# Kernel optimization log

Hardware: AMD Instinct MI355X
Metric: run time of the kernel (lower is better)

The kernel has to match this reference:

```python
import jax, jax.numpy as jnp
import numpy as np


def setup_inputs() -> dict:
    B, N, D, M = 512, 128, 768, 32  # bags, num_class, embed_dim, max bag size
    rng = np.random.default_rng(0)
    sizes = rng.integers(8, 25, size=B)  # variable bag sizes in [8, 24], all <= M
    offsets = np.concatenate([[0], np.cumsum(sizes)]).astype(np.int32)
    nsum = int(offsets[-1])
    scope = np.stack([offsets[:-1], offsets[1:]], axis=1)  # (B, 2) [start, end)

    key = jax.random.key(0)
    k1, k2, k3 = jax.random.split(key, 3)
    rep = jax.random.normal(k1, (nsum, D), dtype=jnp.float32)
    fc_weight = jax.random.normal(k2, (N, D), dtype=jnp.float32) * 0.02
    fc_bias = jax.random.normal(k3, (N,), dtype=jnp.float32) * 0.02
    return {
        "rep": rep,
        "fc_weight": fc_weight,
        "fc_bias": fc_bias,
        "scope": jnp.asarray(scope),
        "max_bag": M,
    }


def reference(rep, fc_weight, fc_bias, scope, max_bag):
    """IntraBagAttention forward (train=False, bag_size=0 branch), ragged bags
    rewritten as padded/masked dense ops.

    rep:       (nsum, D) sentence-encoder outputs
    fc_weight: (N, D), fc_bias: (N,)
    scope:     (B, 2) int [start, end) per bag; max_bag: static int pad bound
    returns:   (B, N) per-relation bag scores
    """
    nsum = rep.shape[0]
    starts = scope[:, 0]
    sizes = scope[:, 1] - scope[:, 0]
    pos = jnp.arange(max_bag)
    idx = jnp.clip(starts[:, None] + pos[None, :], 0, nsum - 1)  # (B, M)
    valid = pos[None, :] < sizes[:, None]                        # (B, M)
    bag = rep[idx]                                               # (B, M, D)

    # att_score = rep @ fc.weight.data.T ; .data => no grad through this use
    w_att = jax.lax.stop_gradient(fc_weight)
    att = jnp.einsum('bmd,nd->bnm', bag, w_att)                  # (B, N, M)
    att = jnp.where(valid[:, None, :], att, -jnp.inf)
    sm = jax.nn.softmax(att, axis=-1)                            # per-bag softmax over sentences

    # weighted segment sum: one attended rep per relation per bag
    rfer = jnp.einsum('bnm,bmd->bnd', sm, bag)                   # (B, N, D)

    # fc(rep_for_each_rel) -> (B, N, N); softmax over classes; take diagonal
    full = jnp.einsum('bnd,kd->bnk', rfer, fc_weight) + fc_bias  # (B, N, N)
    probs = jax.nn.softmax(full, axis=-1)
    return jnp.diagonal(probs, axis1=1, axis2=2)                 # (B, N)
```

## Files before the change

kernel.cpp:

```cpp
#include <hip/hip_runtime.h>
#include <math.h>

#define B_BAGS 512
#define N_REL  128
#define D_DIM  768
#define NCHUNK 4

typedef __attribute__((ext_vector_type(8))) short  bf16x8;
typedef __attribute__((ext_vector_type(4))) float  f32x4;

__device__ inline unsigned pack_hi(float f0, float f1) {
    return __builtin_amdgcn_perm(__float_as_uint(f1), __float_as_uint(f0), 0x07060302u);
}
__device__ inline float trunc_res(float f) {
    return f - __uint_as_float(__float_as_uint(f) & 0xFFFF0000u);
}

__global__ void build_bfrag(const float* __restrict__ W, unsigned* __restrict__ Bfrag) {
    int flat = blockIdx.x * 256 + threadIdx.x;
    int lane = flat & 63;
    int tile = (flat >> 6) & 7;
    int s    = flat >> 9;
    int n  = tile * 16 + (lane & 15);
    int k0 = s * 32 + (lane >> 4) * 8;
    const float* src = &W[n * D_DIM + k0];
    float f[8];
    #pragma unroll
    for (int j = 0; j < 8; ++j) f[j] = src[j];
    unsigned hi[4], lo[4];
    #pragma unroll
    for (int q = 0; q < 4; ++q) {
        hi[q] = pack_hi(f[2*q], f[2*q+1]);
        lo[q] = pack_hi(trunc_res(f[2*q]), trunc_res(f[2*q+1]));
    }
    unsigned base = (unsigned)(((s * 8 + tile) * 2) * 64 + lane) * 4;
    *(uint4*)&Bfrag[base]          = make_uint4(hi[0], hi[1], hi[2], hi[3]);
    *(uint4*)&Bfrag[base + 64 * 4] = make_uint4(lo[0], lo[1], lo[2], lo[3]);
}

__global__ __launch_bounds__(512, 2) void h_gemm(
    const float*    __restrict__ rep,
    const unsigned* __restrict__ Bfrag,
    float*          __restrict__ Hp,
    int nsum, int hstride)
{
    __shared__ unsigned As[2 * 128 * 36];

    const int t     = threadIdx.x;
    const int strip = blockIdx.x;
    const int chunk = blockIdx.y;

    const int wv   = t >> 6;
    const int lane = t & 63;
    const int nl15 = lane & 15;
    const int lg   = lane >> 4;
    const int j    = wv & 3;
    const int nh   = wv >> 2;

    const int srow = t >> 2;
    const int scq  = t & 3;
    int grow = strip * 128 + srow;
    grow = (grow > nsum - 1) ? (nsum - 1) : grow;
    const float* srp = &rep[(size_t)grow * D_DIM + chunk * 192 + scq * 16];

    f32x4 acc[2][4][2];
    #pragma unroll
    for (int mt = 0; mt < 2; ++mt)
        #pragma unroll
        for (int i = 0; i < 4; ++i) {
            acc[mt][i][0] = f32x4{0.f, 0.f, 0.f, 0.f};
            acc[mt][i][1] = f32x4{0.f, 0.f, 0.f, 0.f};
        }

    unsigned afo[2][2];
    #pragma unroll
    for (int mt = 0; mt < 2; ++mt) {
        const int row = (j * 2 + mt) * 16 + nl15;
        afo[mt][0] = (0 * 128 + row) * 36 + lg * 4;
        afo[mt][1] = (1 * 128 + row) * 36 + lg * 4;
    }

    #pragma unroll
    for (int st = 0; st < 3; ++st) {
        if (st) __syncthreads();
        {
            const float4 v0 = *(const float4*)&srp[st * 64];
            const float4 v1 = *(const float4*)&srp[st * 64 + 4];
            const float4 v2 = *(const float4*)&srp[st * 64 + 8];
            const float4 v3 = *(const float4*)&srp[st * 64 + 12];
            unsigned hi[8], lo[8];
            const float f[16] = {v0.x,v0.y,v0.z,v0.w, v1.x,v1.y,v1.z,v1.w,
                                 v2.x,v2.y,v2.z,v2.w, v3.x,v3.y,v3.z,v3.w};
            #pragma unroll
            for (int w = 0; w < 8; ++w) {
                hi[w] = pack_hi(f[2*w], f[2*w+1]);
                lo[w] = pack_hi(trunc_res(f[2*w]), trunc_res(f[2*w+1]));
            }
            const unsigned bh = (0 * 128 + srow) * 36 + scq * 8;
            const unsigned bl = (1 * 128 + srow) * 36 + scq * 8;
            *(uint4*)&As[bh]     = make_uint4(hi[0], hi[1], hi[2], hi[3]);
            *(uint4*)&As[bh + 4] = make_uint4(hi[4], hi[5], hi[6], hi[7]);
            *(uint4*)&As[bl]     = make_uint4(lo[0], lo[1], lo[2], lo[3]);
            *(uint4*)&As[bl + 4] = make_uint4(lo[4], lo[5], lo[6], lo[7]);
        }
        __syncthreads();

        #pragma unroll
        for (int g = 0; g < 2; ++g) {
            const int gsg = chunk * 6 + st * 2 + g;
            bf16x8 ah[2], al[2];
            #pragma unroll
            for (int mt = 0; mt < 2; ++mt) {
                ah[mt] = *(const bf16x8*)&As[afo[mt][0] + g * 16];
                al[mt] = *(const bf16x8*)&As[afo[mt][1] + g * 16];
            }
            #pragma unroll
            for (int i = 0; i < 4; ++i) {
                const int nt = nh * 4 + i;
                const bf16x8 bh = *(const bf16x8*)&Bfrag[((gsg * 8 + nt) * 2 + 0) * 256 + lane * 4];
                const bf16x8 bl = *(const bf16x8*)&Bfrag[((gsg * 8 + nt) * 2 + 1) * 256 + lane * 4];
                #pragma unroll
                for (int mt = 0; mt < 2; ++mt) {
                    acc[mt][i][0] = __builtin_amdgcn_mfma_f32_16x16x32_bf16(ah[mt], bh, acc[mt][i][0], 0, 0, 0);
                    acc[mt][i][1] = __builtin_amdgcn_mfma_f32_16x16x32_bf16(ah[mt], bl, acc[mt][i][1], 0, 0, 0);
                    acc[mt][i][1] = __builtin_amdgcn_mfma_f32_16x16x32_bf16(al[mt], bh, acc[mt][i][1], 0, 0, 0);
                }
            }
        }
    }

    float* H = Hp + (size_t)chunk * hstride;
    #pragma unroll
    for (int mt = 0; mt < 2; ++mt) {
        const int rowb = strip * 128 + (j * 2 + mt) * 16 + lg * 4;
        #pragma unroll
        for (int i = 0; i < 4; ++i) {
            const int col = (nh * 4 + i) * 16 + nl15;
            #pragma unroll
            for (int r = 0; r < 4; ++r)
                H[(size_t)(rowb + r) * N_REL + col] = acc[mt][i][0][r] + acc[mt][i][1][r];
        }
    }
}

__global__ __launch_bounds__(512, 2) void bag_out(
    const float* __restrict__ Hp, int hstride,
    const float* __restrict__ bias,
    const int*   __restrict__ scope,
    float*       __restrict__ out,
    int nsum)
{
    __shared__ unsigned Gfrag[8 * 2 * 64 * 4];
    __shared__ unsigned SMfrag[8 * 2 * 64 * 4];

    const int t = threadIdx.x;
    const int b = blockIdx.x;
    const int start = scope[2 * b];
    const int size  = scope[2 * b + 1] - start;

    const int wv   = t >> 6;
    const int lane = t & 63;
    const int nl15 = lane & 15;
    const int lg   = lane >> 4;
    const int T    = wv;

    float gv[2][4], smv[2][4];
    #pragma unroll
    for (int mt = 0; mt < 2; ++mt)
        #pragma unroll
        for (int r = 0; r < 4; ++r) {
            int row = start + mt * 16 + lg * 4 + r;
            row = (row > nsum - 1) ? (nsum - 1) : row;
            const float* p = &Hp[(size_t)row * N_REL + T * 16 + nl15];
            gv[mt][r] = p[0] + p[(size_t)hstride] + p[(size_t)hstride * 2]
                             + p[(size_t)hstride * 3];
        }

    float vmax = -INFINITY;
    #pragma unroll
    for (int mt = 0; mt < 2; ++mt)
        #pragma unroll
        for (int r = 0; r < 4; ++r) {
            const int m = mt * 16 + lg * 4 + r;
            if (m < size) vmax = fmaxf(vmax, gv[mt][r]);
        }
    vmax = fmaxf(vmax, __shfl_xor(vmax, 16));
    vmax = fmaxf(vmax, __shfl_xor(vmax, 32));

    float ssum = 0.f;
    #pragma unroll
    for (int mt = 0; mt < 2; ++mt)
        #pragma unroll
        for (int r = 0; r < 4; ++r) {
            const int m = mt * 16 + lg * 4 + r;
            float e = (m < size) ? __expf(gv[mt][r] - vmax) : 0.f;
            smv[mt][r] = e;
            ssum += e;
        }
    ssum += __shfl_xor(ssum, 16);
    ssum += __shfl_xor(ssum, 32);
    const float inv = 1.f / ssum;
    #pragma unroll
    for (int mt = 0; mt < 2; ++mt)
        #pragma unroll
        for (int r = 0; r < 4; ++r) smv[mt][r] *= inv;

    #pragma unroll
    for (int mt = 0; mt < 2; ++mt)
        #pragma unroll
        for (int rp = 0; rp < 4; rp += 2) {
            const int m     = mt * 16 + lg * 4 + rp;
            const int lane2 = (m >> 3) * 16 + nl15;
            const int word  = (m >> 1) & 3;
            const int ihi = ((T * 2 + 0) * 64 + lane2) * 4 + word;
            const int ilo = ((T * 2 + 1) * 64 + lane2) * 4 + word;
            Gfrag[ihi]  = pack_hi(gv[mt][rp], gv[mt][rp + 1]);
            Gfrag[ilo]  = pack_hi(trunc_res(gv[mt][rp]), trunc_res(gv[mt][rp + 1]));
            SMfrag[ihi] = pack_hi(smv[mt][rp], smv[mt][rp + 1]);
            SMfrag[ilo] = pack_hi(trunc_res(smv[mt][rp]), trunc_res(smv[mt][rp + 1]));
        }
    __syncthreads();

    float bias_r[8];
    #pragma unroll
    for (int ct = 0; ct < 8; ++ct) bias_r[ct] = bias[ct * 16 + nl15];

    f32x4 facc[8];
    #pragma unroll
    for (int ct = 0; ct < 8; ++ct) facc[ct] = f32x4{0.f, 0.f, 0.f, 0.f};

    const bf16x8 ah2 = *(const bf16x8*)&SMfrag[((T * 2 + 0) * 64 + lane) * 4];
    const bf16x8 al2 = *(const bf16x8*)&SMfrag[((T * 2 + 1) * 64 + lane) * 4];
    #pragma unroll
    for (int ct = 0; ct < 8; ++ct) {
        const bf16x8 bh = *(const bf16x8*)&Gfrag[((ct * 2 + 0) * 64 + lane) * 4];
        const bf16x8 bl = *(const bf16x8*)&Gfrag[((ct * 2 + 1) * 64 + lane) * 4];
        facc[ct] = __builtin_amdgcn_mfma_f32_16x16x32_bf16(ah2, bh, facc[ct], 0, 0, 0);
        facc[ct] = __builtin_amdgcn_mfma_f32_16x16x32_bf16(ah2, bl, facc[ct], 0, 0, 0);
        facc[ct] = __builtin_amdgcn_mfma_f32_16x16x32_bf16(al2, bh, facc[ct], 0, 0, 0);
    }

    #pragma unroll
    for (int r = 0; r < 4; ++r) {
        float s[8];
        #pragma unroll
        for (int ct = 0; ct < 8; ++ct) s[ct] = facc[ct][r] + bias_r[ct];

        float mx = s[0];
        #pragma unroll
        for (int ct = 1; ct < 8; ++ct) mx = fmaxf(mx, s[ct]);
        mx = fmaxf(mx, __shfl_xor(mx, 1));
        mx = fmaxf(mx, __shfl_xor(mx, 2));
        mx = fmaxf(mx, __shfl_xor(mx, 4));
        mx = fmaxf(mx, __shfl_xor(mx, 8));

        float l = 0.f;
        #pragma unroll
        for (int ct = 0; ct < 8; ++ct) l += __expf(s[ct] - mx);
        l += __shfl_xor(l, 1);
        l += __shfl_xor(l, 2);
        l += __shfl_xor(l, 4);
        l += __shfl_xor(l, 8);

        const int nl = lg * 4 + r;
        float sd = s[0];
        #pragma unroll
        for (int ct = 1; ct < 8; ++ct) sd = (ct == T) ? s[ct] : sd;
        if (nl15 == nl) {
            out[b * N_REL + T * 16 + nl] = __expf(sd - mx) / l;
        }
    }
}

extern "C" void kernel_launch(void* const* d_in, const int* in_sizes, int n_in,
                              void* d_out, int out_size, void* d_ws, size_t ws_size,
                              hipStream_t stream) {
    const float* rep   = (const float*)d_in[0];
    const float* W     = (const float*)d_in[1];
    const float* bias  = (const float*)d_in[2];
    const int*   scope = (const int*)d_in[3];

    const int nsum    = in_sizes[0] / D_DIM;
    const int strips  = (nsum + 127) >> 7;
    const int hstride = strips * 128 * N_REL;

    unsigned* Bfrag = (unsigned*)d_ws;
    float*    Hp    = (float*)((char*)d_ws + 393216);

    build_bfrag<<<48, 256, 0, stream>>>(W, Bfrag);
    h_gemm<<<dim3(strips, NCHUNK), 512, 0, stream>>>(rep, Bfrag, Hp, nsum, hstride);
    bag_out<<<B_BAGS, 512, 0, stream>>>(Hp, hstride, bias, scope,
                                        (float*)d_out, nsum);
}
```

Baseline: 100.9 us.

## Replace split-K GEMM with full-K 32-row strips and drop partial-sum reduction

The H GEMM stops splitting K into four chunks with 128-row strips and instead gives each block 32 rows over the full K of 768. Each block now produces final H values directly, so the four partial buffers and the four-way reduction in bag_out go away. That saves the extra partial-sum writes and reads. The cost is less reuse of each B fragment per block, since each wave now covers one 16-row tile and two N tiles, plus a longer serial K loop of six stages with barriers.

```diff
diff --git a/kernel.cpp b/kernel.cpp
--- a/kernel.cpp
+++ b/kernel.cpp
@@ -4,7 +4,6 @@
 #define B_BAGS 512
 #define N_REL  128
 #define D_DIM  768
-#define NCHUNK 4
 
 typedef __attribute__((ext_vector_type(8))) short  bf16x8;
 typedef __attribute__((ext_vector_type(4))) float  f32x4;
@@ -41,110 +40,83 @@
 __global__ __launch_bounds__(512, 2) void h_gemm(
     const float*    __restrict__ rep,
     const unsigned* __restrict__ Bfrag,
-    float*          __restrict__ Hp,
-    int nsum, int hstride)
+    float*          __restrict__ H,
+    int nsum)
 {
-    __shared__ unsigned As[2 * 128 * 36];
+    __shared__ unsigned As[2][32][68];
 
     const int t     = threadIdx.x;
     const int strip = blockIdx.x;
-    const int chunk = blockIdx.y;
 
     const int wv   = t >> 6;
     const int lane = t & 63;
     const int nl15 = lane & 15;
     const int lg   = lane >> 4;
-    const int j    = wv & 3;
-    const int nh   = wv >> 2;
-
-    const int srow = t >> 2;
-    const int scq  = t & 3;
-    int grow = strip * 128 + srow;
+    const int mt   = wv & 1;
+    const int nh   = wv >> 1;
+
+    const int srow = t >> 4;
+    const int scq  = t & 15;
+    int grow = strip * 32 + srow;
     grow = (grow > nsum - 1) ? (nsum - 1) : grow;
-    const float* srp = &rep[(size_t)grow * D_DIM + chunk * 192 + scq * 16];
-
-    f32x4 acc[2][4][2];
-    #pragma unroll
-    for (int mt = 0; mt < 2; ++mt)
-        #pragma unroll
-        for (int i = 0; i < 4; ++i) {
-            acc[mt][i][0] = f32x4{0.f, 0.f, 0.f, 0.f};
-            acc[mt][i][1] = f32x4{0.f, 0.f, 0.f, 0.f};
-        }
-
-    unsigned afo[2][2];
-    #pragma unroll
-    for (int mt = 0; mt < 2; ++mt) {
-        const int row = (j * 2 + mt) * 16 + nl15;
-        afo[mt][0] = (0 * 128 + row) * 36 + lg * 4;
-        afo[mt][1] = (1 * 128 + row) * 36 + lg * 4;
-    }
-
-    #pragma unroll
-    for (int st = 0; st < 3; ++st) {
+    const float* srp = &rep[(size_t)grow * D_DIM + scq * 8];
+
+    f32x4 acc[2][2];
+    #pragma unroll
+    for (int ntl = 0; ntl < 2; ++ntl) {
+        acc[ntl][0] = f32x4{0.f, 0.f, 0.f, 0.f};
+        acc[ntl][1] = f32x4{0.f, 0.f, 0.f, 0.f};
+    }
+
+    const int arow = mt * 16 + nl15;
+
+    #pragma unroll
+    for (int st = 0; st < 6; ++st) {
         if (st) __syncthreads();
         {
-            const float4 v0 = *(const float4*)&srp[st * 64];
-            const float4 v1 = *(const float4*)&srp[st * 64 + 4];
-            const float4 v2 = *(const float4*)&srp[st * 64 + 8];
-            const float4 v3 = *(const float4*)&srp[st * 64 + 12];
-            unsigned hi[8], lo[8];
-            const float f[16] = {v0.x,v0.y,v0.z,v0.w, v1.x,v1.y,v1.z,v1.w,
-                                 v2.x,v2.y,v2.z,v2.w, v3.x,v3.y,v3.z,v3.w};
+            const float4 v0 = *(const float4*)&srp[st * 128];
+            const float4 v1 = *(const float4*)&srp[st * 128 + 4];
+            const float f[8] = {v0.x, v0.y, v0.z, v0.w, v1.x, v1.y, v1.z, v1.w};
+            unsigned hi[4], lo[4];
             #pragma unroll
-            for (int w = 0; w < 8; ++w) {
+            for (int w = 0; w < 4; ++w) {
                 hi[w] = pack_hi(f[2*w], f[2*w+1]);
                 lo[w] = pack_hi(trunc_res(f[2*w]), trunc_res(f[2*w+1]));
             }
-            const unsigned bh = (0 * 128 + srow) * 36 + scq * 8;
-            const unsigned bl = (1 * 128 + srow) * 36 + scq * 8;
-            *(uint4*)&As[bh]     = make_uint4(hi[0], hi[1], hi[2], hi[3]);
-            *(uint4*)&As[bh + 4] = make_uint4(hi[4], hi[5], hi[6], hi[7]);
-            *(uint4*)&As[bl]     = make_uint4(lo[0], lo[1], lo[2], lo[3]);
-            *(uint4*)&As[bl + 4] = make_uint4(lo[4], lo[5], lo[6], lo[7]);
+            *(uint4*)&As[0][srow][scq * 4] = make_uint4(hi[0], hi[1], hi[2], hi[3]);
+            *(uint4*)&As[1][srow][scq * 4] = make_uint4(lo[0], lo[1], lo[2], lo[3]);
         }
         __syncthreads();
 
         #pragma unroll
-        for (int g = 0; g < 2; ++g) {
-            const int gsg = chunk * 6 + st * 2 + g;
-            bf16x8 ah[2], al[2];
+        for (int g = 0; g < 4; ++g) {
+            const int gs = st * 4 + g;
+            const bf16x8 ah = *(const bf16x8*)&As[0][arow][g * 16 + lg * 4];
+            const bf16x8 al = *(const bf16x8*)&As[1][arow][g * 16 + lg * 4];
             #pragma unroll
-            for (int mt = 0; mt < 2; ++mt) {
-                ah[mt] = *(const bf16x8*)&As[afo[mt][0] + g * 16];
-                al[mt] = *(const bf16x8*)&As[afo[mt][1] + g * 16];
+            for (int ntl = 0; ntl < 2; ++ntl) {
+                const int nt = nh * 2 + ntl;
+                const bf16x8 bh = *(const bf16x8*)&Bfrag[((gs * 8 + nt) * 2 + 0) * 256 + lane * 4];
+                const bf16x8 bl = *(const bf16x8*)&Bfrag[((gs * 8 + nt) * 2 + 1) * 256 + lane * 4];
+                acc[ntl][0] = __builtin_amdgcn_mfma_f32_16x16x32_bf16(ah, bh, acc[ntl][0], 0, 0, 0);
+                acc[ntl][1] = __builtin_amdgcn_mfma_f32_16x16x32_bf16(ah, bl, acc[ntl][1], 0, 0, 0);
+                acc[ntl][1] = __builtin_amdgcn_mfma_f32_16x16x32_bf16(al, bh, acc[ntl][1], 0, 0, 0);
             }
-            #pragma unroll
-            for (int i = 0; i < 4; ++i) {
-                const int nt = nh * 4 + i;
-                const bf16x8 bh = *(const bf16x8*)&Bfrag[((gsg * 8 + nt) * 2 + 0) * 256 + lane * 4];
-                const bf16x8 bl = *(const bf16x8*)&Bfrag[((gsg * 8 + nt) * 2 + 1) * 256 + lane * 4];
-                #pragma unroll
-                for (int mt = 0; mt < 2; ++mt) {
-                    acc[mt][i][0] = __builtin_amdgcn_mfma_f32_16x16x32_bf16(ah[mt], bh, acc[mt][i][0], 0, 0, 0);
-                    acc[mt][i][1] = __builtin_amdgcn_mfma_f32_16x16x32_bf16(ah[mt], bl, acc[mt][i][1], 0, 0, 0);
-                    acc[mt][i][1] = __builtin_amdgcn_mfma_f32_16x16x32_bf16(al[mt], bh, acc[mt][i][1], 0, 0, 0);
-                }
-            }
-        }
-    }
-
-    float* H = Hp + (size_t)chunk * hstride;
-    #pragma unroll
-    for (int mt = 0; mt < 2; ++mt) {
-        const int rowb = strip * 128 + (j * 2 + mt) * 16 + lg * 4;
-        #pragma unroll
-        for (int i = 0; i < 4; ++i) {
-            const int col = (nh * 4 + i) * 16 + nl15;
-            #pragma unroll
-            for (int r = 0; r < 4; ++r)
-                H[(size_t)(rowb + r) * N_REL + col] = acc[mt][i][0][r] + acc[mt][i][1][r];
-        }
+        }
+    }
+
+    const int rowb = strip * 32 + mt * 16 + lg * 4;
+    #pragma unroll
+    for (int ntl = 0; ntl < 2; ++ntl) {
+        const int col = (nh * 2 + ntl) * 16 + nl15;
+        #pragma unroll
+        for (int r = 0; r < 4; ++r)
+            H[(size_t)(rowb + r) * N_REL + col] = acc[ntl][0][r] + acc[ntl][1][r];
     }
 }
 
 __global__ __launch_bounds__(512, 2) void bag_out(
-    const float* __restrict__ Hp, int hstride,
+    const float* __restrict__ H,
     const float* __restrict__ bias,
     const int*   __restrict__ scope,
     float*       __restrict__ out,
@@ -171,9 +143,7 @@
         for (int r = 0; r < 4; ++r) {
             int row = start + mt * 16 + lg * 4 + r;
             row = (row > nsum - 1) ? (nsum - 1) : row;
-            const float* p = &Hp[(size_t)row * N_REL + T * 16 + nl15];
-            gv[mt][r] = p[0] + p[(size_t)hstride] + p[(size_t)hstride * 2]
-                             + p[(size_t)hstride * 3];
+            gv[mt][r] = H[(size_t)row * N_REL + T * 16 + nl15];
         }
 
     float vmax = -INFINITY;
@@ -280,15 +250,13 @@
     const float* bias  = (const float*)d_in[2];
     const int*   scope = (const int*)d_in[3];
 
-    const int nsum    = in_sizes[0] / D_DIM;
-    const int strips  = (nsum + 127) >> 7;
-    const int hstride = strips * 128 * N_REL;
+    const int nsum   = in_sizes[0] / D_DIM;
+    const int strips = (nsum + 31) >> 5;
 
     unsigned* Bfrag = (unsigned*)d_ws;
-    float*    Hp    = (float*)((char*)d_ws + 393216);
+    float*    H     = (float*)((char*)d_ws + 393216);
 
     build_bfrag<<<48, 256, 0, stream>>>(W, Bfrag);
-    h_gemm<<<dim3(strips, NCHUNK), 512, 0, stream>>>(rep, Bfrag, Hp, nsum, hstride);
-    bag_out<<<B_BAGS, 512, 0, stream>>>(Hp, hstride, bias, scope,
-                                        (float*)d_out, nsum);
-}
+    h_gemm<<<strips, 512, 0, stream>>>(rep, Bfrag, H, nsum);
+    bag_out<<<B_BAGS, 512, 0, stream>>>(H, bias, scope, (float*)d_out, nsum);
+}
```

Result: faster. 97.53 us (-3.4%).
